# Optimization experiments

Hardware: AMD Instinct MI355X
Metric: run time of the kernel (lower is better)

## Reference

```python
import jax, jax.numpy as jnp
import numpy as np

IN_DIM = 2048
OUT_DIM = 2 * IN_DIM  # 4096
MEM_LEN = 32768
BETA = 5000.0


def setup_inputs() -> dict:
    key = jax.random.key(0)
    k1, k2, k3, k4 = jax.random.split(key, 4)
    return {
        "x": jax.random.normal(k1, (1, IN_DIM), jnp.float32),
        "memory": jax.random.normal(k2, (MEM_LEN, OUT_DIM), jnp.float32),
        "mem_data": jax.random.normal(k3, (MEM_LEN, IN_DIM), jnp.float32),
        "W_enc": (jax.random.normal(k4, (IN_DIM, OUT_DIM), jnp.float32)
                  / np.float32(np.sqrt(IN_DIM))),
        "b_enc": jnp.zeros((OUT_DIM,), jnp.float32),
        "count": 7,
    }


def reference(x, memory, mem_data, W_enc, b_enc, count):
    # mean/std over memory bank data (torch .std uses ddof=1)
    mean = mem_data.mean(axis=0)
    std = mem_data.std(axis=0, ddof=1)
    zero_std = std == 0
    safe_std = jnp.where(zero_std, 1.0, std)
    new = jnp.where(zero_std, 0.0, (x - mean) / safe_std)  # [1, IN_DIM]
    # encoder: Linear + Tanh
    enc = jnp.tanh(new @ W_enc + b_enc)  # [1, OUT_DIM]
    # L1 distance of the query against every memory slot, then min
    dists = jnp.sum(jnp.abs(memory - enc), axis=1)  # [MEM_LEN]
    loss = dists.min()
    # conditional scatter write-back into memory bank at the rolling pointer
    pos = count % MEM_LEN
    do_update = loss <= BETA
    new_memory = jnp.where(do_update, memory.at[pos].set(enc[0]), memory)
    new_mem_data = jnp.where(do_update, mem_data.at[pos].set(x[0]), mem_data)
    return loss, new_memory, new_mem_data
```

## Files before the change

### kernel.cpp

```cpp
#include <hip/hip_runtime.h>

#define IN_DIM   2048
#define OUT_DIM  4096
#define MEM_LEN  32768
#define BETA     5000.0f

#define WS_PS    0
#define WS_PQ    (WS_PS + 128*2048)
#define WS_PG    (WS_PQ + 128*2048)
#define WS_NEW   (WS_PG + 64*4096)
#define WS_ENC   (WS_NEW + 2048)
#define WS_MINB  (WS_ENC + 4096)

__global__ void k_init(float* __restrict__ ws) {
    if (threadIdx.x < 64)
        ((unsigned int*)ws)[WS_MINB + threadIdx.x] = 0x7F800000u;
}

__global__ void k_stats_copy(const float* __restrict__ md,
                             float* __restrict__ out_md,
                             float* __restrict__ ws) {
    const int c  = blockIdx.x * 256 + threadIdx.x;
    const int r0 = blockIdx.y * 256;
    const float* p = md + (size_t)r0 * IN_DIM + c;
    float* o = out_md + (size_t)r0 * IN_DIM + c;
    float s = 0.0f, q = 0.0f;
#pragma unroll 4
    for (int i = 0; i < 256; ++i) {
        float v = __builtin_nontemporal_load(p + (size_t)i * IN_DIM);
        s += v; q += v * v;
        __builtin_nontemporal_store(v, o + (size_t)i * IN_DIM);
    }
    ws[WS_PS + blockIdx.y * IN_DIM + c] = s;
    ws[WS_PQ + blockIdx.y * IN_DIM + c] = q;
}

__global__ void k_new(const float* __restrict__ x, float* __restrict__ ws) {
    int c = blockIdx.x * 256 + threadIdx.x;
    float s = 0.0f, q = 0.0f;
    for (int y = 0; y < 128; ++y) {
        s += ws[WS_PS + y * IN_DIM + c];
        q += ws[WS_PQ + y * IN_DIM + c];
    }
    float mean = s * (1.0f / (float)MEM_LEN);
    float var  = (q - s * mean) * (1.0f / (float)(MEM_LEN - 1));
    float sd   = sqrtf(fmaxf(var, 0.0f));
    ws[WS_NEW + c] = (sd == 0.0f) ? 0.0f : (x[c] - mean) / sd;
}

__global__ void k_gemv(const float* __restrict__ W, float* __restrict__ ws) {
    const int j4 = blockIdx.x * 256 + threadIdx.x;
    const int i0 = blockIdx.y * 32;
    const float4* W4 = (const float4*)W;
    float4 a = make_float4(0.f, 0.f, 0.f, 0.f);
#pragma unroll 8
    for (int k = 0; k < 32; ++k) {
        float nv = ws[WS_NEW + i0 + k];
        float4 w = W4[(size_t)(i0 + k) * 1024 + j4];
        a.x += nv * w.x; a.y += nv * w.y; a.z += nv * w.z; a.w += nv * w.w;
    }
    ((float4*)(ws + WS_PG))[(size_t)blockIdx.y * 1024 + j4] = a;
}

__global__ void k_enc(const float* __restrict__ b_enc, float* __restrict__ ws) {
    int j = blockIdx.x * 256 + threadIdx.x;
    float s = b_enc[j];
    for (int y = 0; y < 64; ++y) s += ws[WS_PG + y * OUT_DIM + j];
    ws[WS_ENC + j] = tanhf(s);
}

__global__ void k_dist_copy(const float* __restrict__ mem,
                            float* __restrict__ out_mem,
                            float* __restrict__ ws) {
    const int lane = threadIdx.x & 63;
    const int wid  = threadIdx.x >> 6;
    const size_t r = (size_t)blockIdx.x * 4 + wid;
    const float* p = mem + r * OUT_DIM;
    float* o = out_mem + r * OUT_DIM;
    float acc = 0.0f;
#pragma unroll 8
    for (int k = 0; k < 64; ++k) {
        int c = k * 64 + lane;
        float m = __builtin_nontemporal_load(p + c);
        acc += fabsf(m - ws[WS_ENC + c]);
        __builtin_nontemporal_store(m, o + c);
    }
    for (int off = 32; off >= 1; off >>= 1)
        acc += __shfl_down(acc, off, 64);
    __shared__ float wmin[4];
    if (lane == 0) wmin[wid] = acc;
    __syncthreads();
    if (threadIdx.x == 0) {
        float b = fminf(fminf(wmin[0], wmin[1]), fminf(wmin[2], wmin[3]));
        atomicMin((unsigned int*)ws + WS_MINB + (blockIdx.x & 63),
                  __float_as_uint(b));
    }
}

__global__ void k_final(const float* __restrict__ x, const int* __restrict__ count,
                        const float* __restrict__ ws, float* __restrict__ d_out) {
    __shared__ float sl;
    int t = threadIdx.x;
    if (t < 64) {
        float v = __uint_as_float(((const unsigned int*)ws)[WS_MINB + t]);
        for (int off = 32; off >= 1; off >>= 1)
            v = fminf(v, __shfl_down(v, off, 64));
        if (t == 0) { d_out[0] = v; sl = v; }
    }
    __syncthreads();
    float loss = sl;
    if (loss <= BETA) {
        int pos = count[0] % MEM_LEN;
        float* outM  = d_out + 1;
        float* outMD = d_out + 1 + (size_t)MEM_LEN * OUT_DIM;
        for (int j = t; j < OUT_DIM; j += 256)
            outM[(size_t)pos * OUT_DIM + j] = ws[WS_ENC + j];
        for (int i = t; i < IN_DIM; i += 256)
            outMD[(size_t)pos * IN_DIM + i] = x[i];
    }
}

extern "C" void kernel_launch(void* const* d_in, const int* in_sizes, int n_in,
                              void* d_out, int out_size, void* d_ws, size_t ws_size,
                              hipStream_t stream) {
    const float* x        = (const float*)d_in[0];
    const float* memory   = (const float*)d_in[1];
    const float* mem_data = (const float*)d_in[2];
    const float* W_enc    = (const float*)d_in[3];
    const float* b_enc    = (const float*)d_in[4];
    const int*   count    = (const int*)d_in[5];
    float* out = (float*)d_out;
    float* ws  = (float*)d_ws;

    float* out_mem = out + 1;
    float* out_md  = out + 1 + (size_t)MEM_LEN * OUT_DIM;

    k_init<<<1, 64, 0, stream>>>(ws);
    k_stats_copy<<<dim3(8, 128), 256, 0, stream>>>(mem_data, out_md, ws);
    k_new<<<8, 256, 0, stream>>>(x, ws);
    k_gemv<<<dim3(4, 64), 256, 0, stream>>>(W_enc, ws);
    k_enc<<<16, 256, 0, stream>>>(b_enc, ws);
    k_dist_copy<<<8192, 256, 0, stream>>>(memory, out_mem, ws);
    k_final<<<1, 256, 0, stream>>>(x, count, ws, out);
}
```

Before: 391.6 us.

## Vectorize streaming copies with float4 loads and shifted aligned stores

Both large streaming copy kernels now load 16-byte vectors. The output sits one float past the input, so each lane gets its predecessor's last element through a wave shuffle and writes an aligned 16-byte store shifted by one element, with edge cases handled separately. The stats grid changes to 2x256 blocks of 128 rows each, and the partial-sum workspace doubles to match. This cuts the number of memory instructions on the bandwidth-bound copies, at the cost of extra shuffles, one scalar load per wave and branchy edge handling.

```diff
diff --git a/kernel.cpp b/kernel.cpp
--- a/kernel.cpp
+++ b/kernel.cpp
@@ -5,9 +5,11 @@
 #define MEM_LEN  32768
 #define BETA     5000.0f
 
+typedef float f4v __attribute__((ext_vector_type(4)));
+
 #define WS_PS    0
-#define WS_PQ    (WS_PS + 128*2048)
-#define WS_PG    (WS_PQ + 128*2048)
+#define WS_PQ    (WS_PS + 256*2048)
+#define WS_PG    (WS_PQ + 256*2048)
 #define WS_NEW   (WS_PG + 64*4096)
 #define WS_ENC   (WS_NEW + 2048)
 #define WS_MINB  (WS_ENC + 4096)
@@ -20,25 +22,38 @@
 __global__ void k_stats_copy(const float* __restrict__ md,
                              float* __restrict__ out_md,
                              float* __restrict__ ws) {
-    const int c  = blockIdx.x * 256 + threadIdx.x;
-    const int r0 = blockIdx.y * 256;
-    const float* p = md + (size_t)r0 * IN_DIM + c;
-    float* o = out_md + (size_t)r0 * IN_DIM + c;
-    float s = 0.0f, q = 0.0f;
+    const int t    = threadIdx.x;
+    const int g    = blockIdx.x * 256 + t;
+    const int lane = t & 63;
+    const int r0   = blockIdx.y * 128;
+    const f4v* in4 = (const f4v*)md;
+    f4v s = {0.f, 0.f, 0.f, 0.f};
+    f4v q = {0.f, 0.f, 0.f, 0.f};
 #pragma unroll 4
-    for (int i = 0; i < 256; ++i) {
-        float v = __builtin_nontemporal_load(p + (size_t)i * IN_DIM);
+    for (int i = 0; i < 128; ++i) {
+        const size_t r = (size_t)(r0 + i);
+        f4v v = __builtin_nontemporal_load(in4 + r * 512 + g);
         s += v; q += v * v;
-        __builtin_nontemporal_store(v, o + (size_t)i * IN_DIM);
+        float pw = __shfl_up(v.w, 1, 64);
+        if (lane == 0 && g > 0)
+            pw = __builtin_nontemporal_load(md + r * IN_DIM + 4 * g - 1);
+        float* orow = out_md + r * IN_DIM;
+        if (g > 0) {
+            f4v o; o.x = pw; o.y = v.x; o.z = v.y; o.w = v.z;
+            __builtin_nontemporal_store(o, (f4v*)(orow + 4 * g - 1));
+        } else {
+            orow[0] = v.x; orow[1] = v.y; orow[2] = v.z;
+        }
+        if (g == 511) orow[IN_DIM - 1] = v.w;
     }
-    ws[WS_PS + blockIdx.y * IN_DIM + c] = s;
-    ws[WS_PQ + blockIdx.y * IN_DIM + c] = q;
+    ((f4v*)(ws + WS_PS))[blockIdx.y * 512 + g] = s;
+    ((f4v*)(ws + WS_PQ))[blockIdx.y * 512 + g] = q;
 }
 
 __global__ void k_new(const float* __restrict__ x, float* __restrict__ ws) {
     int c = blockIdx.x * 256 + threadIdx.x;
     float s = 0.0f, q = 0.0f;
-    for (int y = 0; y < 128; ++y) {
+    for (int y = 0; y < 256; ++y) {
         s += ws[WS_PS + y * IN_DIM + c];
         q += ws[WS_PQ + y * IN_DIM + c];
     }
@@ -51,15 +66,15 @@
 __global__ void k_gemv(const float* __restrict__ W, float* __restrict__ ws) {
     const int j4 = blockIdx.x * 256 + threadIdx.x;
     const int i0 = blockIdx.y * 32;
-    const float4* W4 = (const float4*)W;
-    float4 a = make_float4(0.f, 0.f, 0.f, 0.f);
+    const f4v* W4 = (const f4v*)W;
+    f4v a = {0.f, 0.f, 0.f, 0.f};
 #pragma unroll 8
     for (int k = 0; k < 32; ++k) {
         float nv = ws[WS_NEW + i0 + k];
-        float4 w = W4[(size_t)(i0 + k) * 1024 + j4];
-        a.x += nv * w.x; a.y += nv * w.y; a.z += nv * w.z; a.w += nv * w.w;
+        f4v w = __builtin_nontemporal_load(W4 + (size_t)(i0 + k) * 1024 + j4);
+        a += nv * w;
     }
-    ((float4*)(ws + WS_PG))[(size_t)blockIdx.y * 1024 + j4] = a;
+    ((f4v*)(ws + WS_PG))[(size_t)blockIdx.y * 1024 + j4] = a;
 }
 
 __global__ void k_enc(const float* __restrict__ b_enc, float* __restrict__ ws) {
@@ -75,15 +90,28 @@
     const int lane = threadIdx.x & 63;
     const int wid  = threadIdx.x >> 6;
     const size_t r = (size_t)blockIdx.x * 4 + wid;
-    const float* p = mem + r * OUT_DIM;
-    float* o = out_mem + r * OUT_DIM;
+    const f4v* in4 = (const f4v*)mem + r * 1024;
+    const f4v* e4  = (const f4v*)(ws + WS_ENC);
+    const float* irow = mem + r * OUT_DIM;
+    float* orow = out_mem + r * OUT_DIM;
     float acc = 0.0f;
-#pragma unroll 8
-    for (int k = 0; k < 64; ++k) {
-        int c = k * 64 + lane;
-        float m = __builtin_nontemporal_load(p + c);
-        acc += fabsf(m - ws[WS_ENC + c]);
-        __builtin_nontemporal_store(m, o + c);
+#pragma unroll 4
+    for (int k = 0; k < 16; ++k) {
+        const int g = k * 64 + lane;
+        f4v v = __builtin_nontemporal_load(in4 + g);
+        f4v e = e4[g];
+        acc += fabsf(v.x - e.x) + fabsf(v.y - e.y) +
+               fabsf(v.z - e.z) + fabsf(v.w - e.w);
+        float pw = __shfl_up(v.w, 1, 64);
+        if (lane == 0 && g > 0)
+            pw = __builtin_nontemporal_load(irow + 4 * g - 1);
+        if (g > 0) {
+            f4v o; o.x = pw; o.y = v.x; o.z = v.y; o.w = v.z;
+            __builtin_nontemporal_store(o, (f4v*)(orow + 4 * g - 1));
+        } else {
+            orow[0] = v.x; orow[1] = v.y; orow[2] = v.z;
+        }
+        if (g == 1023) orow[OUT_DIM - 1] = v.w;
     }
     for (int off = 32; off >= 1; off >>= 1)
         acc += __shfl_down(acc, off, 64);
@@ -136,7 +164,7 @@
     float* out_md  = out + 1 + (size_t)MEM_LEN * OUT_DIM;
 
     k_init<<<1, 64, 0, stream>>>(ws);
-    k_stats_copy<<<dim3(8, 128), 256, 0, stream>>>(mem_data, out_md, ws);
+    k_stats_copy<<<dim3(2, 256), 256, 0, stream>>>(mem_data, out_md, ws);
     k_new<<<8, 256, 0, stream>>>(x, ws);
     k_gemv<<<dim3(4, 64), 256, 0, stream>>>(W_enc, ws);
     k_enc<<<16, 256, 0, stream>>>(b_enc, ws);
```

After: 453.6 us. +15.8%, slower.
